# Kernel tuning notes

Measured on AMD Instinct MI355X. Metric: run time of the kernel, lower is better.

Reference implementation:

```python
import jax, jax.numpy as jnp
import numpy as np

HEADS, POINTS = 8, 4
EPS = 1e-5
BS, C, H, W = 2, 256, 200, 200


def _layernorm(x, g, b):
    m = x.mean(-1, keepdims=True)
    v = ((x - m) ** 2).mean(-1, keepdims=True)
    return (x - m) / jnp.sqrt(v + EPS) * g + b


def _sine_pos(bs, Hh, Ww, num_feats, temperature=10000.0):
    # mmdet SinePositionalEncoding with all-zeros mask: cumsum of ones -> 1..H / 1..W
    y = jnp.arange(1, Hh + 1, dtype=jnp.float32)
    x = jnp.arange(1, Ww + 1, dtype=jnp.float32)
    dim_t = jnp.arange(num_feats, dtype=jnp.float32)
    dim_t = temperature ** (2.0 * jnp.floor(dim_t / 2.0) / num_feats)

    def interleave(p):  # p: [N, num_feats] -> [sin(p0),cos(p1),sin(p2),...]
        return jnp.stack((jnp.sin(p[:, 0::2]), jnp.cos(p[:, 1::2])), axis=-1).reshape(p.shape[0], -1)

    pos_x = interleave(x[:, None] / dim_t)  # [W, nf]
    pos_y = interleave(y[:, None] / dim_t)  # [H, nf]
    pos = jnp.concatenate([
        jnp.broadcast_to(pos_y[:, None, :], (Hh, Ww, num_feats)),
        jnp.broadcast_to(pos_x[None, :, :], (Hh, Ww, num_feats)),
    ], axis=-1)  # [H, W, 2*nf] (channel order matches cat((pos_y,pos_x),dim=1) after flatten/permute)
    return jnp.broadcast_to(pos.reshape(1, Hh * Ww, 2 * num_feats), (bs, Hh * Ww, 2 * num_feats))


def _bilinear_sample(v, x, y):
    # v: [bs, heads, H, W, hd]; x, y: [bs, heads, N] pixel coords (align_corners=False, zero padding)
    bs, nh, Hh, Ww, hd = v.shape
    vf = v.reshape(bs, nh, Hh * Ww, hd)
    x0 = jnp.floor(x)
    y0 = jnp.floor(y)
    wx = x - x0
    wy = y - y0

    def gather(xi, yi):
        valid = (xi >= 0) & (xi < Ww) & (yi >= 0) & (yi < Hh)
        xc = jnp.clip(xi, 0, Ww - 1).astype(jnp.int32)
        yc = jnp.clip(yi, 0, Hh - 1).astype(jnp.int32)
        idx = yc * Ww + xc
        g = jnp.take_along_axis(vf, idx[..., None], axis=2)  # [bs, nh, N, hd]
        return g * valid[..., None].astype(v.dtype)

    out = gather(x0, y0) * ((1 - wx) * (1 - wy))[..., None]
    out = out + gather(x0 + 1, y0) * (wx * (1 - wy))[..., None]
    out = out + gather(x0, y0 + 1) * ((1 - wx) * wy)[..., None]
    out = out + gather(x0 + 1, y0 + 1) * (wx * wy)[..., None]
    return out


def _dfa_layer(out, ref, pos, Hh, Ww, p):
    bs, Lq, Cc = out.shape
    hd = Cc // HEADS
    q = out + pos
    value = out @ p['vp_w'].T + p['vp_b']  # [bs, Lq, C]
    off = (q @ p['off_w'].T + p['off_b']).reshape(bs, Lq, HEADS, POINTS, 2)
    aw = jax.nn.softmax((q @ p['aw_w'].T + p['aw_b']).reshape(bs, Lq, HEADS, POINTS), axis=-1)
    norm = jnp.array([Ww, Hh], dtype=out.dtype)
    loc = ref[None, :, None, None, :] + off / norm  # [bs, Lq, heads, P, 2] normalized [0,1]
    x = loc[..., 0] * Ww - 0.5
    y = loc[..., 1] * Hh - 0.5
    v = value.reshape(bs, Lq, HEADS, hd).transpose(0, 2, 1, 3).reshape(bs, HEADS, Hh, Ww, hd)
    xt = x.transpose(0, 2, 1, 3).reshape(bs, HEADS, Lq * POINTS)
    yt = y.transpose(0, 2, 1, 3).reshape(bs, HEADS, Lq * POINTS)
    samp = _bilinear_sample(v, xt, yt).reshape(bs, HEADS, Lq, POINTS, hd)
    attn = jnp.einsum('bhqpd,bqhp->bqhd', samp, aw).reshape(bs, Lq, Cc)
    attn = attn @ p['op_w'].T + p['op_b']
    out = _layernorm(out + attn, p['ln1_g'], p['ln1_b'])
    ffn = jax.nn.relu(out @ p['l1_w'].T + p['l1_b']) @ p['l2_w'].T + p['l2_b']
    return _layernorm(out + ffn, p['ln2_g'], p['ln2_b'])


def setup_inputs() -> dict:
    key = jax.random.key(0)
    ks = jax.random.split(key, 20)
    s = 0.02
    L = 3
    return {
        'bev_feat': jax.random.normal(ks[0], (BS, C, H, W), jnp.float32),
        'proj_q_w': jax.random.normal(ks[1], (C, C), jnp.float32) * s,
        'proj_q_b': jax.random.normal(ks[2], (C,), jnp.float32) * s,
        'off_w': jax.random.normal(ks[3], (L, HEADS * POINTS * 2, C), jnp.float32) * s,
        'off_b': jax.random.normal(ks[4], (L, HEADS * POINTS * 2), jnp.float32) * s,
        'aw_w': jax.random.normal(ks[5], (L, HEADS * POINTS, C), jnp.float32) * s,
        'aw_b': jax.random.normal(ks[6], (L, HEADS * POINTS), jnp.float32) * s,
        'vp_w': jax.random.normal(ks[7], (L, C, C), jnp.float32) * s,
        'vp_b': jax.random.normal(ks[8], (L, C), jnp.float32) * s,
        'op_w': jax.random.normal(ks[9], (L, C, C), jnp.float32) * s,
        'op_b': jax.random.normal(ks[10], (L, C), jnp.float32) * s,
        'ln1_g': jnp.ones((L, C), jnp.float32),
        'ln1_b': jnp.zeros((L, C), jnp.float32),
        'l1_w': jax.random.normal(ks[11], (L, C, C), jnp.float32) * s,
        'l1_b': jax.random.normal(ks[12], (L, C), jnp.float32) * s,
        'l2_w': jax.random.normal(ks[13], (L, C, C), jnp.float32) * s,
        'l2_b': jax.random.normal(ks[14], (L, C), jnp.float32) * s,
        'ln2_g': jnp.ones((L, C), jnp.float32),
        'ln2_b': jnp.zeros((L, C), jnp.float32),
    }


def reference(bev_feat, proj_q_w, proj_q_b, off_w, off_b, aw_w, aw_b, vp_w, vp_b,
              op_w, op_b, ln1_g, ln1_b, l1_w, l1_b, l2_w, l2_b, ln2_g, ln2_b):
    bs, Cc, Hh, Ww = bev_feat.shape
    x = bev_feat.reshape(bs, Cc, Hh * Ww).transpose(0, 2, 1)  # [bs, HW, C]
    out = x @ proj_q_w.T + proj_q_b
    # reference points: pixel centers normalized to [0,1]
    ry, rx = jnp.meshgrid(jnp.linspace(0.5, Hh - 0.5, Hh) / Hh,
                          jnp.linspace(0.5, Ww - 0.5, Ww) / Ww, indexing='ij')
    ref = jnp.stack([rx.reshape(-1), ry.reshape(-1)], axis=-1).astype(bev_feat.dtype)  # [HW, 2]
    pos = _sine_pos(bs, Hh, Ww, Cc // 2).astype(bev_feat.dtype)
    n_layers = off_w.shape[0]
    for i in range(n_layers):
        p = dict(off_w=off_w[i], off_b=off_b[i], aw_w=aw_w[i], aw_b=aw_b[i],
                 vp_w=vp_w[i], vp_b=vp_b[i], op_w=op_w[i], op_b=op_b[i],
                 ln1_g=ln1_g[i], ln1_b=ln1_b[i], l1_w=l1_w[i], l1_b=l1_b[i],
                 l2_w=l2_w[i], l2_b=l2_b[i], ln2_g=ln2_g[i], ln2_b=ln2_b[i])
        out = _dfa_layer(out, ref, pos, Hh, Ww, p)
    return out.transpose(0, 2, 1).reshape(bs, Cc, Hh, Ww)
```

## Files before the change

### kernel.cpp

```cpp
#include <hip/hip_runtime.h>
#include <math.h>

#define HEADS 8
#define POINTS 4
#define BSZ 2
#define CDIM 256
#define HH 200
#define WW 200
#define LQ (HH * WW)
#define MTOT (BSZ * LQ)
#define NLAYERS 3

typedef __attribute__((ext_vector_type(8))) short shortx8;
typedef __attribute__((ext_vector_type(4))) float floatx4;

__device__ __forceinline__ ushort f2b(float f) {
    union { float f; unsigned u; } v; v.f = f;
    unsigned r = v.u + 0x7fffu + ((v.u >> 16) & 1u);
    return (ushort)(r >> 16);
}
__device__ __forceinline__ float b2f(ushort b) {
    union { unsigned u; float f; } v; v.u = ((unsigned)b) << 16;
    return v.f;
}
__device__ __forceinline__ float bitsf(unsigned u) {
    union { unsigned u; float f; } v; v.u = u;
    return v.f;
}
__device__ __forceinline__ uint packbf(float lo, float hi) {
    return (uint)f2b(lo) | ((uint)f2b(hi) << 16);
}

__device__ __forceinline__ int permc(int c) {
    return (c & ~63) | (((c & 15) << 2) | ((c & 63) >> 4));
}
__device__ __forceinline__ int iperm(int p) {
    return (p & ~63) | (((p & 3) << 4) | ((p & 63) >> 2));
}

__global__ __launch_bounds__(256)
void cvt_kernel(const float* __restrict__ in, ushort* __restrict__ out)
{
    const int i = (blockIdx.x * 256 + threadIdx.x) * 4;
    const float4 v = *(const float4*)(in + i);
    ushort4 o;
    o.x = f2b(v.x); o.y = f2b(v.y); o.z = f2b(v.z); o.w = f2b(v.w);
    *(ushort4*)(out + i) = o;
}

__global__ __launch_bounds__(256)
void cvt_perm_kernel(const float* __restrict__ in, ushort* __restrict__ out)
{
    const int idx = (blockIdx.x * 256 + threadIdx.x) * 4;
    const int rowb = idx & ~255;
    const int p0 = idx & 255;
    ushort4 o;
    o.x = f2b(in[rowb + iperm(p0 + 0)]);
    o.y = f2b(in[rowb + iperm(p0 + 1)]);
    o.z = f2b(in[rowb + iperm(p0 + 2)]);
    o.w = f2b(in[rowb + iperm(p0 + 3)]);
    *(ushort4*)(out + idx) = o;
}

__global__ __launch_bounds__(256)
void build_offaw(const float* __restrict__ offw, const float* __restrict__ offb,
                 const float* __restrict__ aww, const float* __restrict__ awb,
                 ushort* __restrict__ wout, float* __restrict__ bout)
{
    const int blk = blockIdx.x;
    const int i = blk >> 7;
    const int r = blk & 127;
    const int c = threadIdx.x;
    float v = 0.f;
    if (r < 64)      v = offw[((size_t)i * 64 + r) * CDIM + c];
    else if (r < 96) v = aww[((size_t)i * 32 + (r - 64)) * CDIM + c];
    wout[((size_t)i * 128 + r) * CDIM + permc(c)] = f2b(v);
    if (c == 0) {
        float bb = 0.f;
        if (r < 64)      bb = offb[i * 64 + r];
        else if (r < 96) bb = awb[i * 32 + (r - 64)];
        bout[i * 128 + r] = bb;
    }
}

__global__ __launch_bounds__(256)
void pos_kernel(ushort* __restrict__ pos)
{
    const int idx = blockIdx.x * 256 + threadIdx.x;
    const int c = idx & 255;
    const int l = idx >> 8;
    const int cc = c & 127;
    const float coord = (c < 128) ? (float)(l / WW + 1) : (float)(l % WW + 1);
    const float expo = (float)(2 * (cc >> 1)) * (1.0f / 128.0f);
    const float t = powf(10000.0f, expo);
    const float ph = coord / t;
    pos[(size_t)l * CDIM + permc(c)] = f2b((cc & 1) ? cosf(ph) : sinf(ph));
}

__global__ __launch_bounds__(256)
void bevT_kernel(const float* __restrict__ in, ushort* __restrict__ out)
{
    __shared__ float tile[32][33];
    const int b = blockIdx.z;
    const int l0 = blockIdx.x * 32;
    const int c0 = blockIdx.y * 32;
    const float* ib = in + (size_t)b * CDIM * LQ;
    ushort* ob = out + (size_t)b * LQ * CDIM;
    #pragma unroll
    for (int j = 0; j < 32; j += 8)
        tile[threadIdx.y + j][threadIdx.x] =
            ib[(size_t)(c0 + threadIdx.y + j) * LQ + l0 + threadIdx.x];
    __syncthreads();
    #pragma unroll
    for (int j = 0; j < 32; j += 8)
        ob[(size_t)(l0 + threadIdx.y + j) * CDIM + c0 + threadIdx.x] =
            f2b(tile[threadIdx.x][threadIdx.y + j]);
}

#define LSTR 40

template<bool RELU, bool F32OUT, bool BF16OUT, bool QOUT>
__global__ __launch_bounds__(256)
void mfma_gemm(const ushort* __restrict__ A, const ushort* __restrict__ B,
               const float* __restrict__ bias,
               float* __restrict__ Cf, ushort* __restrict__ Cb,
               ushort* __restrict__ Cq, const ushort* __restrict__ posb,
               int N, int K)
{
    __shared__ ushort As[128 * LSTR];
    __shared__ ushort Bs[128 * LSTR];
    const int tid = threadIdx.x;
    const int lane = tid & 63;
    const int wave = tid >> 6;
    const int wr = (wave >> 1) * 64;
    const int wc = (wave & 1) * 64;
    const int rowBase = blockIdx.y * 128;
    const int colBase = blockIdx.x * 128;

    floatx4 acc[4][4];
    #pragma unroll
    for (int i = 0; i < 4; i++)
        #pragma unroll
        for (int j = 0; j < 4; j++) {
            floatx4 z = {0.f, 0.f, 0.f, 0.f};
            acc[i][j] = z;
        }

    const int strow = tid >> 2;
    const int stcol = (tid & 3) * 8;
    const int kq = (lane >> 4) * 8;
    const int lr = lane & 15;

    for (int k0 = 0; k0 < K; k0 += 32) {
        #pragma unroll
        for (int j = 0; j < 2; j++) {
            const int r = j * 64 + strow;
            const uint4 av = *(const uint4*)(A + (size_t)(rowBase + r) * K + k0 + stcol);
            const uint4 bv = *(const uint4*)(B + (size_t)(colBase + r) * K + k0 + stcol);
            *(uint4*)(As + r * LSTR + stcol) = av;
            *(uint4*)(Bs + r * LSTR + stcol) = bv;
        }
        __syncthreads();
        shortx8 af[4], bfr[4];
        #pragma unroll
        for (int t = 0; t < 4; t++) {
            af[t]  = *(const shortx8*)(As + (wr + t * 16 + lr) * LSTR + kq);
            bfr[t] = *(const shortx8*)(Bs + (wc + t * 16 + lr) * LSTR + kq);
        }
        #pragma unroll
        for (int mt = 0; mt < 4; mt++)
            #pragma unroll
            for (int nt = 0; nt < 4; nt++)
                acc[mt][nt] = __builtin_amdgcn_mfma_f32_16x16x32_bf16(
                    af[mt], bfr[nt], acc[mt][nt], 0, 0, 0);
        __syncthreads();
    }

    const int colB = colBase + wc + lr;
    const int rowB = rowBase + wr + (lane >> 4) * 4;
    #pragma unroll
    for (int mt = 0; mt < 4; mt++) {
        #pragma unroll
        for (int r = 0; r < 4; r++) {
            const int m = rowB + mt * 16 + r;
            const int pr = (m >= LQ) ? m - LQ : m;
            #pragma unroll
            for (int nt = 0; nt < 4; nt++) {
                const int n = colB + nt * 16;
                float v = acc[mt][nt][r] + bias[n];
                if (RELU) v = fmaxf(v, 0.f);
                if (F32OUT) Cf[(size_t)m * N + n] = v;
                if (BF16OUT) Cb[(size_t)m * N + n] = f2b(v);
                if (QOUT) {
                    const float pv = b2f(posb[(size_t)pr * CDIM + n]);
                    Cq[(size_t)m * N + n] = f2b(v + pv);
                }
            }
        }
    }
}

template<bool RELU, bool LN, bool F32OUT, bool BF16OUT, bool QOUT, bool PERMC>
__global__ __launch_bounds__(256)
void gemm_fused(const ushort* __restrict__ A, const ushort* __restrict__ B,
                const float* __restrict__ bias,
                float* __restrict__ resid, ushort* __restrict__ Cb,
                ushort* __restrict__ Cq, const ushort* __restrict__ posb,
                const float* __restrict__ g, const float* __restrict__ beta)
{
    __shared__ ushort As[64 * LSTR];
    __shared__ ushort Bs[256 * LSTR];

    const int tid = threadIdx.x;
    const int lane = tid & 63;
    const int wave = tid >> 6;
    const int lr = lane & 15;
    const int hi = lane >> 4;
    const int rowBase = blockIdx.x * 64;
    const int wc = wave * 64;

    floatx4 acc[4][4];
    #pragma unroll
    for (int i = 0; i < 4; i++)
        #pragma unroll
        for (int j = 0; j < 4; j++) {
            floatx4 z = {0.f, 0.f, 0.f, 0.f};
            acc[i][j] = z;
        }

    const int strow = tid >> 2;
    const int stcol = (tid & 3) * 8;
    const int kq = hi * 8;

    const ushort* ag = A + (size_t)(rowBase + strow) * CDIM + stcol;
    const ushort* bg = B + (size_t)strow * CDIM + stcol;

    for (int k0 = 0; k0 < CDIM; k0 += 32) {
        const uint4 av  = *(const uint4*)(ag + k0);
        const uint4 bv0 = *(const uint4*)(bg + k0);
        const uint4 bv1 = *(const uint4*)(bg + k0 + 64 * CDIM);
        const uint4 bv2 = *(const uint4*)(bg + k0 + 128 * CDIM);
        const uint4 bv3 = *(const uint4*)(bg + k0 + 192 * CDIM);
        *(uint4*)(As + strow * LSTR + stcol) = av;
        *(uint4*)(Bs + strow * LSTR + stcol) = bv0;
        *(uint4*)(Bs + (strow + 64) * LSTR + stcol) = bv1;
        *(uint4*)(Bs + (strow + 128) * LSTR + stcol) = bv2;
        *(uint4*)(Bs + (strow + 192) * LSTR + stcol) = bv3;
        __syncthreads();
        shortx8 af[4], bfr[4];
        #pragma unroll
        for (int t = 0; t < 4; t++) {
            af[t]  = *(const shortx8*)(As + (t * 16 + lr) * LSTR + kq);
            bfr[t] = *(const shortx8*)(Bs + (wc + t * 16 + lr) * LSTR + kq);
        }
        #pragma unroll
        for (int mt = 0; mt < 4; mt++)
            #pragma unroll
            for (int nt = 0; nt < 4; nt++)
                acc[mt][nt] = __builtin_amdgcn_mfma_f32_16x16x32_bf16(
                    af[mt], bfr[nt], acc[mt][nt], 0, 0, 0);
        __syncthreads();
    }

    float bcol[4];
    #pragma unroll
    for (int nt = 0; nt < 4; nt++) bcol[nt] = bias[wc + nt * 16 + lr];

    if (LN) {
        float2 (*red)[4] = (float2(*)[4])As;
        #pragma unroll
        for (int mt = 0; mt < 4; mt++) {
            #pragma unroll
            for (int r = 0; r < 4; r++) {
                const int mrel = mt * 16 + hi * 4 + r;
                const int m = rowBase + mrel;
                const float4 rv = *(const float4*)(resid + (size_t)m * CDIM + wc + lr * 4);
                float s = 0.f, sq = 0.f;
                #pragma unroll
                for (int nt = 0; nt < 4; nt++) {
                    float x = acc[mt][nt][r] + bcol[nt] + (&rv.x)[nt];
                    acc[mt][nt][r] = x;
                    s += x; sq += x * x;
                }
                #pragma unroll
                for (int o = 8; o >= 1; o >>= 1) {
                    s  += __shfl_xor(s, o, 64);
                    sq += __shfl_xor(sq, o, 64);
                }
                if (lr == 0) { float2 t2; t2.x = s; t2.y = sq; red[mrel][wave] = t2; }
            }
        }
        __syncthreads();
        float gcol[4], btcol[4];
        #pragma unroll
        for (int nt = 0; nt < 4; nt++) {
            gcol[nt]  = g[wc + nt * 16 + lr];
            btcol[nt] = beta[wc + nt * 16 + lr];
        }
        #pragma unroll
        for (int mt = 0; mt < 4; mt++) {
            #pragma unroll
            for (int r = 0; r < 4; r++) {
                const int mrel = mt * 16 + hi * 4 + r;
                const int m = rowBase + mrel;
                const float2 t0 = red[mrel][0], t1 = red[mrel][1];
                const float2 t2 = red[mrel][2], t3 = red[mrel][3];
                const float S  = (t0.x + t1.x) + (t2.x + t3.x);
                const float SQ = (t0.y + t1.y) + (t2.y + t3.y);
                const float mean = S * (1.0f / CDIM);
                const float var = SQ * (1.0f / CDIM) - mean * mean;
                const float rstd = rsqrtf(var + 1e-5f);
                const int pr = (m >= LQ) ? m - LQ : m;
                float4 wv;
                ushort4 ob, qq;
                ushort4 pp;
                if (QOUT) pp = *(const ushort4*)(posb + (size_t)pr * CDIM + wc + lr * 4);
                #pragma unroll
                for (int nt = 0; nt < 4; nt++) {
                    const float y = (acc[mt][nt][r] - mean) * rstd * gcol[nt] + btcol[nt];
                    (&wv.x)[nt] = y;
                    if (BF16OUT) (&ob.x)[nt] = f2b(y);
                    if (QOUT)    (&qq.x)[nt] = f2b(y + b2f((&pp.x)[nt]));
                }
                *(float4*)(resid + (size_t)m * CDIM + wc + lr * 4) = wv;
                if (BF16OUT) *(ushort4*)(Cb + (size_t)m * CDIM + wc + lr * 4) = ob;
                if (QOUT)    *(ushort4*)(Cq + (size_t)m * CDIM + wc + lr * 4) = qq;
            }
        }
    } else {
        #pragma unroll
        for (int mt = 0; mt < 4; mt++) {
            #pragma unroll
            for (int r = 0; r < 4; r++) {
                const int m = rowBase + mt * 16 + hi * 4 + r;
                const int pr = (m >= LQ) ? m - LQ : m;
                float4 wv;
                ushort4 ob, qq, pp;
                if (QOUT && PERMC)
                    pp = *(const ushort4*)(posb + (size_t)pr * CDIM + wc + lr * 4);
                #pragma unroll
                for (int nt = 0; nt < 4; nt++) {
                    float y = acc[mt][nt][r] + bcol[nt];
                    if (RELU) y = fmaxf(y, 0.f);
                    (&wv.x)[nt] = y;
                    if (PERMC) {
                        if (BF16OUT) (&ob.x)[nt] = f2b(y);
                        if (QOUT)    (&qq.x)[nt] = f2b(y + b2f((&pp.x)[nt]));
                    } else {
                        const int col = wc + nt * 16 + lr;
                        if (BF16OUT) Cb[(size_t)m * CDIM + col] = f2b(y);
                        if (QOUT) Cq[(size_t)m * CDIM + col] =
                            f2b(y + b2f(posb[(size_t)pr * CDIM + col]));
                    }
                }
                if (F32OUT) *(float4*)(resid + (size_t)m * CDIM + wc + lr * 4) = wv;
                if (PERMC && BF16OUT)
                    *(ushort4*)(Cb + (size_t)m * CDIM + wc + lr * 4) = ob;
                if (PERMC && QOUT)
                    *(ushort4*)(Cq + (size_t)m * CDIM + wc + lr * 4) = qq;
            }
        }
    }
}

__global__ __launch_bounds__(256)
void sample_kernel(const ushort* __restrict__ val,
                   const float* __restrict__ offaw,
                   ushort* __restrict__ attn)
{
    const int tid = threadIdx.x;
    const int m = blockIdx.x * 8 + (tid >> 5);
    const int lane = tid & 31;
    const int head = lane >> 2;
    const int c = head * 32 + (lane & 3) * 8;
    const int b = (m >= LQ) ? 1 : 0;
    const int l = m - (b ? LQ : 0);

    const float* row = offaw + (size_t)m * 128;
    const float4 lg  = *(const float4*)(row + 64 + head * 4);
    const float4 o01 = *(const float4*)(row + head * 8);
    const float4 o23 = *(const float4*)(row + head * 8 + 4);

    const float mx = fmaxf(fmaxf(lg.x, lg.y), fmaxf(lg.z, lg.w));
    const float e0 = expf(lg.x - mx), e1 = expf(lg.y - mx);
    const float e2 = expf(lg.z - mx), e3 = expf(lg.w - mx);
    const float inv = 1.0f / (e0 + e1 + e2 + e3);
    const float awv[4] = {e0 * inv, e1 * inv, e2 * inv, e3 * inv};

    const float lx = (float)(l % WW);
    const float ly = (float)(l / WW);
    const float px[4] = {lx + o01.x, lx + o01.z, lx + o23.x, lx + o23.z};
    const float py[4] = {ly + o01.y, ly + o01.w, ly + o23.y, ly + o23.w};

    const ushort* vb = val + (size_t)b * LQ * CDIM;
    uint4 cv[16];
    float cw[16];
    #pragma unroll
    for (int p = 0; p < POINTS; p++) {
        const float x = px[p], y = py[p];
        const float xf = floorf(x), yf = floorf(y);
        const int x0 = (int)xf, y0 = (int)yf;
        const float wx = x - xf, wy = y - yf;
        const int x0c = min(max(x0, 0), WW - 1);
        const int x1c = min(max(x0 + 1, 0), WW - 1);
        const int y0c = min(max(y0, 0), HH - 1);
        const int y1c = min(max(y0 + 1, 0), HH - 1);
        const float vx0 = (x0 >= 0 && x0 < WW) ? 1.f : 0.f;
        const float vx1 = (x0 + 1 >= 0 && x0 + 1 < WW) ? 1.f : 0.f;
        const float vy0 = (y0 >= 0 && y0 < HH) ? 1.f : 0.f;
        const float vy1 = (y0 + 1 >= 0 && y0 + 1 < HH) ? 1.f : 0.f;
        const float a = awv[p];
        cw[p * 4 + 0] = a * (1.f - wx) * (1.f - wy) * vx0 * vy0;
        cw[p * 4 + 1] = a * wx * (1.f - wy) * vx1 * vy0;
        cw[p * 4 + 2] = a * (1.f - wx) * wy * vx0 * vy1;
        cw[p * 4 + 3] = a * wx * wy * vx1 * vy1;
        const int r0 = y0c * WW, r1 = y1c * WW;
        cv[p * 4 + 0] = *(const uint4*)(vb + (((unsigned)(r0 + x0c)) << 8) + c);
        cv[p * 4 + 1] = *(const uint4*)(vb + (((unsigned)(r0 + x1c)) << 8) + c);
        cv[p * 4 + 2] = *(const uint4*)(vb + (((unsigned)(r1 + x0c)) << 8) + c);
        cv[p * 4 + 3] = *(const uint4*)(vb + (((unsigned)(r1 + x1c)) << 8) + c);
    }
    float a0 = 0.f, a1 = 0.f, a2 = 0.f, a3 = 0.f;
    float a4 = 0.f, a5 = 0.f, a6 = 0.f, a7 = 0.f;
    #pragma unroll
    for (int i = 0; i < 16; i++) {
        const float wgt = cw[i];
        a0 = fmaf(wgt, bitsf(cv[i].x << 16), a0);
        a1 = fmaf(wgt, bitsf(cv[i].x & 0xffff0000u), a1);
        a2 = fmaf(wgt, bitsf(cv[i].y << 16), a2);
        a3 = fmaf(wgt, bitsf(cv[i].y & 0xffff0000u), a3);
        a4 = fmaf(wgt, bitsf(cv[i].z << 16), a4);
        a5 = fmaf(wgt, bitsf(cv[i].z & 0xffff0000u), a5);
        a6 = fmaf(wgt, bitsf(cv[i].w << 16), a6);
        a7 = fmaf(wgt, bitsf(cv[i].w & 0xffff0000u), a7);
    }
    uint4 o;
    o.x = packbf(a0, a1); o.y = packbf(a2, a3);
    o.z = packbf(a4, a5); o.w = packbf(a6, a7);
    *(uint4*)(attn + (size_t)m * CDIM + c) = o;
}

__global__ __launch_bounds__(256)
void transpose_out(const float* __restrict__ in, float* __restrict__ outp)
{
    __shared__ float tile[32][33];
    const int b = blockIdx.z;
    const int l0 = blockIdx.x * 32;
    const int c0 = blockIdx.y * 32;
    const float* ib = in + (size_t)b * LQ * CDIM;
    float* ob = outp + (size_t)b * CDIM * LQ;
    #pragma unroll
    for (int j = 0; j < 32; j += 8)
        tile[threadIdx.y + j][threadIdx.x] =
            ib[(size_t)(l0 + threadIdx.y + j) * CDIM + c0 + threadIdx.x];
    __syncthreads();
    #pragma unroll
    for (int j = 0; j < 32; j += 8)
        ob[(size_t)iperm(c0 + threadIdx.y + j) * LQ + l0 + threadIdx.x] =
            tile[threadIdx.x][threadIdx.y + j];
}

extern "C" void kernel_launch(void* const* d_in, const int* in_sizes, int n_in,
                              void* d_out, int out_size, void* d_ws, size_t ws_size,
                              hipStream_t stream)
{
    const float* bev      = (const float*)d_in[0];
    const float* proj_q_w = (const float*)d_in[1];
    const float* proj_q_b = (const float*)d_in[2];
    const float* off_w    = (const float*)d_in[3];
    const float* off_b    = (const float*)d_in[4];
    const float* aw_w     = (const float*)d_in[5];
    const float* aw_b     = (const float*)d_in[6];
    const float* vp_w     = (const float*)d_in[7];
    const float* vp_b     = (const float*)d_in[8];
    const float* op_w     = (const float*)d_in[9];
    const float* op_b     = (const float*)d_in[10];
    const float* ln1_g    = (const float*)d_in[11];
    const float* ln1_b    = (const float*)d_in[12];
    const float* l1_w     = (const float*)d_in[13];
    const float* l1_b     = (const float*)d_in[14];
    const float* l2_w     = (const float*)d_in[15];
    const float* l2_b     = (const float*)d_in[16];
    const float* ln2_g    = (const float*)d_in[17];
    const float* ln2_b    = (const float*)d_in[18];
    float* outp = (float*)d_out;

    char* w = (char*)d_ws;
    float*  out_f   = (float*)(w);
    float*  offaw_f = (float*)(w + 81920000);
    ushort* out_b   = (ushort*)(w + 163840000);
    ushort* q_b     = (ushort*)(w + 204800000);
    ushort* val_b   = (ushort*)(w + 245760000);
    ushort* pos_b   = (ushort*)(w + 286720000);
    ushort* w_b     = (ushort*)(w + 307200000);
    ushort* wproj = w_b;
    ushort* wvp   = w_b + 65536;
    ushort* wop   = w_b + 65536 + 196608;
    ushort* wl1   = w_b + 65536 + 2 * 196608;
    ushort* wl2   = w_b + 65536 + 3 * 196608;
    ushort* wofa  = w_b + 65536 + 4 * 196608;
    float*  bofa  = (float*)(w + 307200000 + 2 * (65536 + 4 * 196608 + 98304));

    const dim3 blk(256);

    cvt_kernel<<<dim3(65536 / 1024), blk, 0, stream>>>(proj_q_w, wproj);
    cvt_perm_kernel<<<dim3(196608 / 1024), blk, 0, stream>>>(vp_w, wvp);
    cvt_kernel<<<dim3(196608 / 1024), blk, 0, stream>>>(op_w, wop);
    cvt_perm_kernel<<<dim3(196608 / 1024), blk, 0, stream>>>(l1_w, wl1);
    cvt_perm_kernel<<<dim3(196608 / 1024), blk, 0, stream>>>(l2_w, wl2);
    build_offaw<<<dim3(3 * 128), blk, 0, stream>>>(off_w, off_b, aw_w, aw_b, wofa, bofa);
    pos_kernel<<<dim3((LQ * CDIM) / 256), blk, 0, stream>>>(pos_b);
    bevT_kernel<<<dim3(LQ / 32, CDIM / 32, BSZ), dim3(32, 8), 0, stream>>>(bev, val_b);

    const dim3 gF(MTOT / 64);
    const dim3 g128(1, MTOT / 128);

    gemm_fused<false, false, true, true, true, true><<<gF, blk, 0, stream>>>(
        val_b, wproj, proj_q_b, out_f, out_b, q_b, pos_b, nullptr, nullptr);

    for (int i = 0; i < NLAYERS; i++) {
        gemm_fused<false, false, false, true, false, false><<<gF, blk, 0, stream>>>(
            out_b, wvp + (size_t)i * 65536, vp_b + (size_t)i * CDIM,
            nullptr, val_b, nullptr, nullptr, nullptr, nullptr);
        mfma_gemm<false, true, false, false><<<g128, blk, 0, stream>>>(
            q_b, wofa + (size_t)i * 32768, bofa + (size_t)i * 128,
            offaw_f, nullptr, nullptr, nullptr, 128, CDIM);
        sample_kernel<<<dim3(MTOT / 8), blk, 0, stream>>>(val_b, offaw_f, q_b);
        gemm_fused<false, true, false, true, false, true><<<gF, blk, 0, stream>>>(
            q_b, wop + (size_t)i * 65536, op_b + (size_t)i * CDIM,
            out_f, out_b, nullptr, pos_b,
            ln1_g + (size_t)i * CDIM, ln1_b + (size_t)i * CDIM);
        gemm_fused<true, false, false, true, false, true><<<gF, blk, 0, stream>>>(
            out_b, wl1 + (size_t)i * 65536, l1_b + (size_t)i * CDIM,
            nullptr, val_b, nullptr, nullptr, nullptr, nullptr);
        if (i < NLAYERS - 1) {
            gemm_fused<false, true, false, true, true, true><<<gF, blk, 0, stream>>>(
                val_b, wl2 + (size_t)i * 65536, l2_b + (size_t)i * CDIM,
                out_f, out_b, q_b, pos_b,
                ln2_g + (size_t)i * CDIM, ln2_b + (size_t)i * CDIM);
        } else {
            gemm_fused<false, true, false, false, false, true><<<gF, blk, 0, stream>>>(
                val_b, wl2 + (size_t)i * 65536, l2_b + (size_t)i * CDIM,
                out_f, nullptr, nullptr, pos_b,
                ln2_g + (size_t)i * CDIM, ln2_b + (size_t)i * CDIM);
        }
    }

    transpose_out<<<dim3(LQ / 32, CDIM / 32, BSZ), dim3(32, 8), 0, stream>>>(out_f, outp);
}
```

Measured before the change: 1.026 ms.

## Double-buffer LDS in fused GEMM and widen tile to 128 rows with 512 threads

The fused GEMM now uses 512-thread blocks with 8 waves arranged 2x4, covering 128 rows per block. This halves the number of blocks and lets each block reuse the full 256-column B tile across twice as many rows. The K loop ping-pongs between two shared-memory buffers, so the global loads for the next K slice overlap the current MFMAs, and one barrier per iteration is removed. The cost is twice the shared memory per block and higher register pressure under the new launch bounds, which may lower occupancy.

Result: slower. 1.181 ms (+15.2%).

```diff
diff --git a/kernel.cpp b/kernel.cpp
--- a/kernel.cpp
+++ b/kernel.cpp
@@ -201,23 +201,24 @@
 }
 
 template<bool RELU, bool LN, bool F32OUT, bool BF16OUT, bool QOUT, bool PERMC>
-__global__ __launch_bounds__(256)
+__global__ __launch_bounds__(512, 4)
 void gemm_fused(const ushort* __restrict__ A, const ushort* __restrict__ B,
                 const float* __restrict__ bias,
                 float* __restrict__ resid, ushort* __restrict__ Cb,
                 ushort* __restrict__ Cq, const ushort* __restrict__ posb,
                 const float* __restrict__ g, const float* __restrict__ beta)
 {
-    __shared__ ushort As[64 * LSTR];
-    __shared__ ushort Bs[256 * LSTR];
+    __shared__ ushort As[2][128 * LSTR];
+    __shared__ ushort Bs[2][256 * LSTR];
 
     const int tid = threadIdx.x;
     const int lane = tid & 63;
     const int wave = tid >> 6;
     const int lr = lane & 15;
     const int hi = lane >> 4;
-    const int rowBase = blockIdx.x * 64;
-    const int wc = wave * 64;
+    const int rowBase = blockIdx.x * 128;
+    const int wr = (wave >> 2) * 64;
+    const int wc = (wave & 3) * 64;
 
     floatx4 acc[4][4];
     #pragma unroll
@@ -235,23 +236,31 @@
     const ushort* ag = A + (size_t)(rowBase + strow) * CDIM + stcol;
     const ushort* bg = B + (size_t)strow * CDIM + stcol;
 
-    for (int k0 = 0; k0 < CDIM; k0 += 32) {
-        const uint4 av  = *(const uint4*)(ag + k0);
-        const uint4 bv0 = *(const uint4*)(bg + k0);
-        const uint4 bv1 = *(const uint4*)(bg + k0 + 64 * CDIM);
-        const uint4 bv2 = *(const uint4*)(bg + k0 + 128 * CDIM);
-        const uint4 bv3 = *(const uint4*)(bg + k0 + 192 * CDIM);
-        *(uint4*)(As + strow * LSTR + stcol) = av;
-        *(uint4*)(Bs + strow * LSTR + stcol) = bv0;
-        *(uint4*)(Bs + (strow + 64) * LSTR + stcol) = bv1;
-        *(uint4*)(Bs + (strow + 128) * LSTR + stcol) = bv2;
-        *(uint4*)(Bs + (strow + 192) * LSTR + stcol) = bv3;
+    {
+        const uint4 av  = *(const uint4*)(ag);
+        const uint4 bv0 = *(const uint4*)(bg);
+        const uint4 bv1 = *(const uint4*)(bg + 128 * CDIM);
+        *(uint4*)(As[0] + strow * LSTR + stcol) = av;
+        *(uint4*)(Bs[0] + strow * LSTR + stcol) = bv0;
+        *(uint4*)(Bs[0] + (strow + 128) * LSTR + stcol) = bv1;
+    }
+
+    #pragma unroll
+    for (int kt = 0; kt < 8; ++kt) {
+        const int p = kt & 1;
         __syncthreads();
+        uint4 av, bv0, bv1;
+        if (kt < 7) {
+            const int ko = (kt + 1) * 32;
+            av  = *(const uint4*)(ag + ko);
+            bv0 = *(const uint4*)(bg + ko);
+            bv1 = *(const uint4*)(bg + ko + 128 * CDIM);
+        }
         shortx8 af[4], bfr[4];
         #pragma unroll
         for (int t = 0; t < 4; t++) {
-            af[t]  = *(const shortx8*)(As + (t * 16 + lr) * LSTR + kq);
-            bfr[t] = *(const shortx8*)(Bs + (wc + t * 16 + lr) * LSTR + kq);
+            af[t]  = *(const shortx8*)(As[p] + (wr + t * 16 + lr) * LSTR + kq);
+            bfr[t] = *(const shortx8*)(Bs[p] + (wc + t * 16 + lr) * LSTR + kq);
         }
         #pragma unroll
         for (int mt = 0; mt < 4; mt++)
@@ -259,20 +268,25 @@
             for (int nt = 0; nt < 4; nt++)
                 acc[mt][nt] = __builtin_amdgcn_mfma_f32_16x16x32_bf16(
                     af[mt], bfr[nt], acc[mt][nt], 0, 0, 0);
-        __syncthreads();
-    }
+        if (kt < 7) {
+            *(uint4*)(As[p ^ 1] + strow * LSTR + stcol) = av;
+            *(uint4*)(Bs[p ^ 1] + strow * LSTR + stcol) = bv0;
+            *(uint4*)(Bs[p ^ 1] + (strow + 128) * LSTR + stcol) = bv1;
+        }
+    }
+    __syncthreads();
 
     float bcol[4];
     #pragma unroll
     for (int nt = 0; nt < 4; nt++) bcol[nt] = bias[wc + nt * 16 + lr];
 
     if (LN) {
-        float2 (*red)[4] = (float2(*)[4])As;
+        float2 (*red)[4] = (float2(*)[4])As[0];
         #pragma unroll
         for (int mt = 0; mt < 4; mt++) {
             #pragma unroll
             for (int r = 0; r < 4; r++) {
-                const int mrel = mt * 16 + hi * 4 + r;
+                const int mrel = wr + mt * 16 + hi * 4 + r;
                 const int m = rowBase + mrel;
                 const float4 rv = *(const float4*)(resid + (size_t)m * CDIM + wc + lr * 4);
                 float s = 0.f, sq = 0.f;
@@ -287,7 +301,7 @@
                     s  += __shfl_xor(s, o, 64);
                     sq += __shfl_xor(sq, o, 64);
                 }
-                if (lr == 0) { float2 t2; t2.x = s; t2.y = sq; red[mrel][wave] = t2; }
+                if (lr == 0) { float2 t2; t2.x = s; t2.y = sq; red[mrel][wave & 3] = t2; }
             }
         }
         __syncthreads();
@@ -301,7 +315,7 @@
         for (int mt = 0; mt < 4; mt++) {
             #pragma unroll
             for (int r = 0; r < 4; r++) {
-                const int mrel = mt * 16 + hi * 4 + r;
+                const int mrel = wr + mt * 16 + hi * 4 + r;
                 const int m = rowBase + mrel;
                 const float2 t0 = red[mrel][0], t1 = red[mrel][1];
                 const float2 t2 = red[mrel][2], t3 = red[mrel][3];
@@ -332,7 +346,7 @@
         for (int mt = 0; mt < 4; mt++) {
             #pragma unroll
             for (int r = 0; r < 4; r++) {
-                const int m = rowBase + mt * 16 + hi * 4 + r;
+                const int m = rowBase + wr + mt * 16 + hi * 4 + r;
                 const int pr = (m >= LQ) ? m - LQ : m;
                 float4 wv;
                 ushort4 ob, qq, pp;
@@ -502,6 +516,7 @@
     float*  bofa  = (float*)(w + 307200000 + 2 * (65536 + 4 * 196608 + 98304));
 
     const dim3 blk(256);
+    const dim3 blk512(512);
 
     cvt_kernel<<<dim3(65536 / 1024), blk, 0, stream>>>(proj_q_w, wproj);
     cvt_perm_kernel<<<dim3(196608 / 1024), blk, 0, stream>>>(vp_w, wvp);
@@ -512,34 +527,34 @@
     pos_kernel<<<dim3((LQ * CDIM) / 256), blk, 0, stream>>>(pos_b);
     bevT_kernel<<<dim3(LQ / 32, CDIM / 32, BSZ), dim3(32, 8), 0, stream>>>(bev, val_b);
 
-    const dim3 gF(MTOT / 64);
+    const dim3 gF(MTOT / 128);
     const dim3 g128(1, MTOT / 128);
 
-    gemm_fused<false, false, true, true, true, true><<<gF, blk, 0, stream>>>(
+    gemm_fused<false, false, true, true, true, true><<<gF, blk512, 0, stream>>>(
         val_b, wproj, proj_q_b, out_f, out_b, q_b, pos_b, nullptr, nullptr);
 
     for (int i = 0; i < NLAYERS; i++) {
-        gemm_fused<false, false, false, true, false, false><<<gF, blk, 0, stream>>>(
+        gemm_fused<false, false, false, true, false, false><<<gF, blk512, 0, stream>>>(
             out_b, wvp + (size_t)i * 65536, vp_b + (size_t)i * CDIM,
             nullptr, val_b, nullptr, nullptr, nullptr, nullptr);
         mfma_gemm<false, true, false, false><<<g128, blk, 0, stream>>>(
             q_b, wofa + (size_t)i * 32768, bofa + (size_t)i * 128,
             offaw_f, nullptr, nullptr, nullptr, 128, CDIM);
         sample_kernel<<<dim3(MTOT / 8), blk, 0, stream>>>(val_b, offaw_f, q_b);
-        gemm_fused<false, true, false, true, false, true><<<gF, blk, 0, stream>>>(
+        gemm_fused<false, true, false, true, false, true><<<gF, blk512, 0, stream>>>(
             q_b, wop + (size_t)i * 65536, op_b + (size_t)i * CDIM,
             out_f, out_b, nullptr, pos_b,
             ln1_g + (size_t)i * CDIM, ln1_b + (size_t)i * CDIM);
-        gemm_fused<true, false, false, true, false, true><<<gF, blk, 0, stream>>>(
+        gemm_fused<true, false, false, true, false, true><<<gF, blk512, 0, stream>>>(
             out_b, wl1 + (size_t)i * 65536, l1_b + (size_t)i * CDIM,
             nullptr, val_b, nullptr, nullptr, nullptr, nullptr);
         if (i < NLAYERS - 1) {
-            gemm_fused<false, true, false, true, true, true><<<gF, blk, 0, stream>>>(
+            gemm_fused<false, true, false, true, true, true><<<gF, blk512, 0, stream>>>(
                 val_b, wl2 + (size_t)i * 65536, l2_b + (size_t)i * CDIM,
                 out_f, out_b, q_b, pos_b,
                 ln2_g + (size_t)i * CDIM, ln2_b + (size_t)i * CDIM);
         } else {
-            gemm_fused<false, true, false, false, false, true><<<gF, blk, 0, stream>>>(
+            gemm_fused<false, true, false, false, false, true><<<gF, blk512, 0, stream>>>(
                 val_b, wl2 + (size_t)i * 65536, l2_b + (size_t)i * CDIM,
                 out_f, nullptr, nullptr, pos_b,
                 ln2_g + (size_t)i * CDIM, ln2_b + (size_t)i * CDIM);
```
